# Kernel tuning notes

Measured on AMD Instinct MI355X. Metric: run time of the kernel, lower is better.

Reference implementation:

```python
import jax, jax.numpy as jnp
import numpy as np

MODEL_DIMS = 2048
BATCH, SEQ = 4, 4096
NFREQ = MODEL_DIMS // 2 + 1  # rfft spectrum length


def setup_inputs() -> dict:
    key = jax.random.key(0)
    k1, k2, k3, k4 = jax.random.split(key, 4)
    x = jax.random.normal(k1, (BATCH, SEQ, MODEL_DIMS), dtype=jnp.float32)
    queries = jax.random.normal(k2, (1, 1, NFREQ), dtype=jnp.float32)
    keyvalues = jax.random.normal(k3, (1, 1, NFREQ), dtype=jnp.float32)
    # torch nn.Linear(model_dims, model_dims, bias=False): weight is [out, in]
    w_out = jax.random.normal(k4, (MODEL_DIMS, MODEL_DIMS), dtype=jnp.float32) * (MODEL_DIMS ** -0.5)
    return {"x": x, "queries": queries, "keyvalues": keyvalues, "w_out": w_out}


def reference(x, queries, keyvalues, w_out):
    # hrr.fft = rfft over feature dim -> complex64 [B, S, NFREQ]
    xhat = jnp.fft.rfft(x, axis=-1)
    q = xhat * queries            # real spectral params broadcast-multiply
    kv = xhat * keyvalues
    kv = jnp.cumsum(kv, axis=1)   # causal prefix sum over sequence
    qv = q * kv
    values_hat = jnp.fft.irfft(qv, n=x.shape[-1], axis=-1)  # back to real [B, S, D]
    # torch Linear: y = x @ W^T
    return jnp.einsum('bsd,ed->bse', values_hat, w_out)
```

## Files before the change

kernel.cpp:

```cpp
#include <hip/hip_runtime.h>
#include <hip/hip_bf16.h>
#include <stdint.h>

#define BATCH 4
#define SEQ   4096
#define DIM   2048
#define NFREQ 1025
#define NCPLX 1024
#define ROWS  (BATCH*SEQ)

#define SCH  16
#define NSC  (SEQ/SCH)
#define NSCG 16
#define NGRP (NSC/NSCG)

#define SPEC_STRIDE 257

typedef __bf16 bf16x8 __attribute__((ext_vector_type(8)));
typedef float  f32x4  __attribute__((ext_vector_type(4)));

__device__ __forceinline__ int drev4(int n) {
  return ((n&3)<<8) | (((n>>2)&3)<<6) | (((n>>4)&3)<<4) | (((n>>6)&3)<<2) | ((n>>8)&3);
}
#define ZI(i) ((i) + ((i)>>4))

__device__ __forceinline__ float2 cmulf(float2 a, float2 b) {
  return make_float2(a.x*b.x - a.y*b.y, a.x*b.y + a.y*b.x);
}

__device__ __forceinline__ unsigned short f2bf(float f) {
  union { float f; unsigned u; } v; v.f = f;
  unsigned r = v.u + 0x7fffu + ((v.u >> 16) & 1u);
  return (unsigned short)(r >> 16);
}
__device__ __forceinline__ unsigned packbf(float2 v) {
  return (unsigned)f2bf(v.x) | ((unsigned)f2bf(v.y) << 16);
}
__device__ __forceinline__ float2 unpackbf(unsigned u) {
  union { unsigned u; float f; } a, b;
  a.u = u << 16; b.u = u & 0xffff0000u;
  return make_float2(a.f, b.f);
}

template<int INV>
__device__ __forceinline__ void fft_stages_tw(float2* z, int tid, const float2* tw1) {
  {
    int b4 = tid*4;
    float2 x0=z[ZI(b4)], x1=z[ZI(b4+1)], x2=z[ZI(b4+2)], x3=z[ZI(b4+3)];
    float2 a = make_float2(x0.x+x2.x, x0.y+x2.y), b = make_float2(x0.x-x2.x, x0.y-x2.y);
    float2 c = make_float2(x1.x+x3.x, x1.y+x3.y), d = make_float2(x1.x-x3.x, x1.y-x3.y);
    z[ZI(b4)]   = make_float2(a.x+c.x, a.y+c.y);
    z[ZI(b4+2)] = make_float2(a.x-c.x, a.y-c.y);
    if (!INV) { z[ZI(b4+1)] = make_float2(b.x+d.y, b.y-d.x);
                z[ZI(b4+3)] = make_float2(b.x-d.y, b.y+d.x); }
    else      { z[ZI(b4+1)] = make_float2(b.x-d.y, b.y+d.x);
                z[ZI(b4+3)] = make_float2(b.x+d.y, b.y-d.x); }
  }
  __syncthreads();
#pragma unroll
  for (int s = 0; s < 4; ++s) {
    const int lq = 2 + 2*s;
    const int q  = 1 << lq;
    int j = tid & (q-1), g = tid >> lq;
    int base = (g << (lq+2)) + j;
    float2 w1 = tw1[s]; if (INV) w1.y = -w1.y;
    float2 w2 = cmulf(w1, w1), w3 = cmulf(w2, w1);
    float2 x0 = z[ZI(base)];
    float2 x1 = cmulf(z[ZI(base+q)],   w1);
    float2 x2 = cmulf(z[ZI(base+2*q)], w2);
    float2 x3 = cmulf(z[ZI(base+3*q)], w3);
    float2 a = make_float2(x0.x+x2.x, x0.y+x2.y), b = make_float2(x0.x-x2.x, x0.y-x2.y);
    float2 c = make_float2(x1.x+x3.x, x1.y+x3.y), d = make_float2(x1.x-x3.x, x1.y-x3.y);
    z[ZI(base)]     = make_float2(a.x+c.x, a.y+c.y);
    z[ZI(base+2*q)] = make_float2(a.x-c.x, a.y-c.y);
    if (!INV) { z[ZI(base+q)]   = make_float2(b.x+d.y, b.y-d.x);
                z[ZI(base+3*q)] = make_float2(b.x-d.y, b.y+d.x); }
    else      { z[ZI(base+q)]   = make_float2(b.x-d.y, b.y+d.x);
                z[ZI(base+3*q)] = make_float2(b.x+d.y, b.y-d.x); }
    __syncthreads();
  }
}

__device__ __forceinline__ void make_tw1(int tid, float2* tw1) {
#pragma unroll
  for (int s = 0; s < 4; ++s) {
    const int lq = 2 + 2*s;
    const int q  = 1 << lq;
    int j = tid & (q-1);
    float ang = -6.2831853071795864769f * (float)j / (float)(4*q);
    float sw, cw; __sincosf(ang, &sw, &cw);
    tw1[s] = make_float2(cw, sw);
  }
}

__global__ __launch_bounds__(256) void fwd_fused(const float* __restrict__ x,
                                                 const float* __restrict__ kvs,
                                                 uint4* __restrict__ spec,
                                                 float2* __restrict__ partial) {
  __shared__ float2 z[ZI(1023)+2];
  const int tid = threadIdx.x;
  const int sc = blockIdx.x & (NSC-1), b = blockIdx.x >> 8;

  float2 tw1[4];
  make_tw1(tid, tw1);
  const int kA = tid, kB = tid + 256;
  float swA, cwA, swB, cwB;
  __sincosf(-3.14159265358979323846f * (float)kA / 1024.0f, &swA, &cwA);
  __sincosf(-3.14159265358979323846f * (float)kB / 1024.0f, &swB, &cwB);
  int id0 = ZI(drev4(2*tid)),     id1 = ZI(drev4(2*tid+1));
  int id2 = ZI(drev4(2*tid+512)), id3 = ZI(drev4(2*tid+513));

  float2 sA={0,0}, sAp={0,0}, sB={0,0}, sBp={0,0}, s5={0,0};

  const size_t row0 = (size_t)b*SEQ + (size_t)sc*SCH;
  const float* xrow = x + row0*DIM;
  float4 c0 = ((const float4*)xrow)[tid];
  float4 c1 = ((const float4*)xrow)[tid + 256];

  for (int s = 0; s < SCH; ++s) {
    float4 n0f, n1f;
    if (s+1 < SCH) {
      const float* nx = xrow + (size_t)(s+1)*DIM;
      n0f = ((const float4*)nx)[tid]; n1f = ((const float4*)nx)[tid + 256];
    }
    z[id0] = make_float2(c0.x, c0.y); z[id1] = make_float2(c0.z, c0.w);
    z[id2] = make_float2(c1.x, c1.y); z[id3] = make_float2(c1.z, c1.w);
    __syncthreads();
    fft_stages_tw<0>(z, tid, tw1);
    float2 ZkA = z[ZI(kA)], ZnA = z[ZI((NCPLX - kA) & (NCPLX-1))];
    float2 ZkB = z[ZI(kB)], ZnB = z[ZI(768 - tid)];
    float Er = 0.5f*(ZkA.x + ZnA.x), Ei = 0.5f*(ZkA.y - ZnA.y);
    float dr = 0.5f*(ZkA.x - ZnA.x), di = 0.5f*(ZkA.y + ZnA.y);
    float2 vA  = make_float2( Er + cwA*di + swA*dr,  Ei + swA*di - cwA*dr);
    float2 vAp = make_float2( Er - cwA*di - swA*dr, -Ei + swA*di - cwA*dr);
    float Fr = 0.5f*(ZkB.x + ZnB.x), Fi = 0.5f*(ZkB.y - ZnB.y);
    float er = 0.5f*(ZkB.x - ZnB.x), ei = 0.5f*(ZkB.y + ZnB.y);
    float2 vB  = make_float2( Fr + cwB*ei + swB*er,  Fi + swB*ei - cwB*er);
    float2 vBp = make_float2( Fr - cwB*ei - swB*er, -Fi + swB*ei - cwB*er);
    sA.x += vA.x;  sA.y += vA.y;   sAp.x += vAp.x; sAp.y += vAp.y;
    sB.x += vB.x;  sB.y += vB.y;   sBp.x += vBp.x; sBp.y += vBp.y;
    uint4* sprow = spec + (row0 + s) * SPEC_STRIDE;
    sprow[tid] = make_uint4(packbf(vA), packbf(vAp), packbf(vB), packbf(vBp));
    if (tid == 0) {
      float2 Z5 = z[ZI(512)];
      float2 v5 = make_float2(Z5.x, -Z5.y);
      s5.x += v5.x; s5.y += v5.y;
      ((unsigned*)(sprow + 256))[0] = packbf(v5);
    }
    __syncthreads();
    c0 = n0f; c1 = n1f;
  }
  float2* pp = partial + ((size_t)(b*NSC + sc)) * NFREQ;
  float kvA = kvs[kA], kvAp = kvs[NCPLX - kA], kvB = kvs[kB], kvBp = kvs[768 - tid];
  pp[kA]          = make_float2(kvA*sA.x,  kvA*sA.y);
  pp[NCPLX - kA]  = make_float2(kvAp*sAp.x, kvAp*sAp.y);
  pp[kB]          = make_float2(kvB*sB.x,  kvB*sB.y);
  pp[768 - tid]   = make_float2(kvBp*sBp.x, kvBp*sBp.y);
  if (tid == 0) { float kv5 = kvs[512]; pp[512] = make_float2(kv5*s5.x, kv5*s5.y); }
}

__global__ __launch_bounds__(256) void wfft(const float* __restrict__ w,
                                            unsigned short* __restrict__ H) {
  __shared__ float2 z[ZI(1023)+2];
  __shared__ __align__(16) unsigned short hrow[2048];
  const int tid = threadIdx.x;
  const int e = blockIdx.x;

  float2 tw1[4];
  make_tw1(tid, tw1);
  const int kB = tid + 256;
  float swA, cwA, swB, cwB;
  __sincosf(-3.14159265358979323846f * (float)tid / 1024.0f, &swA, &cwA);
  __sincosf(-3.14159265358979323846f * (float)kB  / 1024.0f, &swB, &cwB);
  int id0 = ZI(drev4(2*tid)),     id1 = ZI(drev4(2*tid+1));
  int id2 = ZI(drev4(2*tid+512)), id3 = ZI(drev4(2*tid+513));

  const float* wr = w + (size_t)e * DIM;
  float4 c0 = ((const float4*)wr)[tid];
  float4 c1 = ((const float4*)wr)[tid + 256];
  z[id0] = make_float2(c0.x, c0.y); z[id1] = make_float2(c0.z, c0.w);
  z[id2] = make_float2(c1.x, c1.y); z[id3] = make_float2(c1.z, c1.w);
  __syncthreads();
  fft_stages_tw<0>(z, tid, tw1);

  float2 ZkA = z[ZI(tid)], ZnA = z[ZI((NCPLX - tid) & (NCPLX-1))];
  float2 ZkB = z[ZI(kB)],  ZnB = z[ZI(768 - tid)];
  float Er = 0.5f*(ZkA.x + ZnA.x), Ei = 0.5f*(ZkA.y - ZnA.y);
  float dr = 0.5f*(ZkA.x - ZnA.x), di = 0.5f*(ZkA.y + ZnA.y);
  float2 vA  = make_float2( Er + cwA*di + swA*dr,  Ei + swA*di - cwA*dr);
  float2 vAp = make_float2( Er - cwA*di - swA*dr, -Ei + swA*di - cwA*dr);
  float Fr = 0.5f*(ZkB.x + ZnB.x), Fi = 0.5f*(ZkB.y - ZnB.y);
  float er = 0.5f*(ZkB.x - ZnB.x), ei = 0.5f*(ZkB.y + ZnB.y);
  float2 vB  = make_float2( Fr + cwB*ei + swB*er,  Fi + swB*ei - cwB*er);
  float2 vBp = make_float2( Fr - cwB*ei - swB*er, -Fi + swB*ei - cwB*er);

  const float invN = 1.0f/2048.0f, twoN = 2.0f/2048.0f;
  float aA  = (tid == 0) ? invN : twoN;
  float aAp = (tid == 0) ? invN : twoN;
  hrow[tid]        = f2bf(aA  * vA.x);
  hrow[1024 - tid] = f2bf(aAp * vAp.x);
  hrow[256 + tid]  = f2bf(twoN * vB.x);
  hrow[768 - tid]  = f2bf(twoN * vBp.x);
  if (tid) {
    hrow[1024 + tid] = f2bf(twoN * vA.y);
    hrow[2048 - tid] = f2bf(twoN * vAp.y);
  }
  hrow[1280 + tid] = f2bf(twoN * vB.y);
  hrow[1792 - tid] = f2bf(twoN * vBp.y);
  if (tid == 0) {
    float2 Z5 = z[ZI(512)];
    hrow[512]  = f2bf(twoN * Z5.x);
    hrow[1536] = f2bf(twoN * (-Z5.y));
  }
  __syncthreads();
  ((uint4*)(H + (size_t)e * DIM))[tid] = ((const uint4*)hrow)[tid];
}

__global__ __launch_bounds__(256) void scanA(float2* __restrict__ partial,
                                             float2* __restrict__ gtot) {
  int kc = blockIdx.x % 5, g = (blockIdx.x / 5) % NGRP, b = blockIdx.x / (5*NGRP);
  int k = kc*256 + threadIdx.x;
  if (k >= NFREQ) return;
  float2* p = partial + ((size_t)(b*NSC + g*NSCG)) * NFREQ + k;
  float2 run = {0.f, 0.f};
#pragma unroll
  for (int i = 0; i < NSCG; ++i) {
    float2 t = p[(size_t)i*NFREQ];
    p[(size_t)i*NFREQ] = run;
    run.x += t.x; run.y += t.y;
  }
  gtot[((size_t)(b*NGRP + g)) * NFREQ + k] = run;
}

__global__ __launch_bounds__(256) void scanB(float2* __restrict__ gtot) {
  int kc = blockIdx.x % 5, b = blockIdx.x / 5;
  int k = kc*256 + threadIdx.x;
  if (k >= NFREQ) return;
  float2* p = gtot + ((size_t)b*NGRP) * NFREQ + k;
  float2 run = {0.f, 0.f};
#pragma unroll
  for (int g = 0; g < NGRP; ++g) {
    float2 t = p[(size_t)g*NFREQ];
    p[(size_t)g*NFREQ] = run;
    run.x += t.x; run.y += t.y;
  }
}

__global__ __launch_bounds__(256) void inv_fused(const uint4* __restrict__ spec,
                                                 const float* __restrict__ kvs,
                                                 const float* __restrict__ qs_,
                                                 const float2* __restrict__ partial,
                                                 const float2* __restrict__ gtot,
                                                 unsigned short* __restrict__ G) {
  __shared__ __align__(16) unsigned short grow[2048];
  const int tid = threadIdx.x;
  const int sc = blockIdx.x & (NSC-1), b = blockIdx.x >> 8;
  const int kA = tid, kB = tid + 256;

  float ksA = kvs[kA], ksAp = kvs[NCPLX - kA], ksB = kvs[kB], ksBp = kvs[768 - tid];
  float qsA = qs_[kA], qsAp = qs_[NCPLX - kA], qsB = qs_[kB], qsBp = qs_[768 - tid];

  const float2* pp = partial + ((size_t)(b*NSC + sc)) * NFREQ;
  const float2* gp = gtot + ((size_t)(b*NGRP + (sc >> 4))) * NFREQ;
  float2 CA  = make_float2(pp[kA].x + gp[kA].x,                 pp[kA].y + gp[kA].y);
  float2 CAp = make_float2(pp[NCPLX-kA].x + gp[NCPLX-kA].x,     pp[NCPLX-kA].y + gp[NCPLX-kA].y);
  float2 CB  = make_float2(pp[kB].x + gp[kB].x,                 pp[kB].y + gp[kB].y);
  float2 CBp = make_float2(pp[768-tid].x + gp[768-tid].x,       pp[768-tid].y + gp[768-tid].y);
  float ks5 = kvs[512], qs5 = qs_[512];
  float2 C5 = make_float2(pp[512].x + gp[512].x, pp[512].y + gp[512].y);

  const size_t row0 = (size_t)b*SEQ + (size_t)sc*SCH;
  const uint4* sprow = spec + row0 * SPEC_STRIDE;
  uint4 sp = sprow[tid];
  unsigned spN = ((const unsigned*)(sprow + 256))[0];

  for (int s = 0; s < SCH; ++s) {
    uint4 spn; unsigned spNn;
    if (s+1 < SCH) {
      const uint4* nr = sprow + (size_t)(s+1) * SPEC_STRIDE;
      spn = nr[tid]; spNn = ((const unsigned*)(nr + 256))[0];
    }
    float2 vA = unpackbf(sp.x), vAp = unpackbf(sp.y);
    float2 vB = unpackbf(sp.z), vBp = unpackbf(sp.w);
    CA.x  += vA.x*ksA;   CA.y  += vA.y*ksA;
    CAp.x += vAp.x*ksAp; CAp.y += vAp.y*ksAp;
    CB.x  += vB.x*ksB;   CB.y  += vB.y*ksB;
    CBp.x += vBp.x*ksBp; CBp.y += vBp.y*ksBp;
    float2 qvA  = make_float2(qsA *(vA.x*CA.x  - vA.y*CA.y),  qsA *(vA.x*CA.y  + vA.y*CA.x));
    float2 qvAp = make_float2(qsAp*(vAp.x*CAp.x- vAp.y*CAp.y),qsAp*(vAp.x*CAp.y+ vAp.y*CAp.x));
    float2 qvB  = make_float2(qsB *(vB.x*CB.x  - vB.y*CB.y),  qsB *(vB.x*CB.y  + vB.y*CB.x));
    float2 qvBp = make_float2(qsBp*(vBp.x*CBp.x- vBp.y*CBp.y),qsBp*(vBp.x*CBp.y+ vBp.y*CBp.x));
    grow[tid]        = f2bf(qvA.x);
    grow[1024 - tid] = f2bf(qvAp.x);
    grow[256 + tid]  = f2bf(qvB.x);
    grow[768 - tid]  = f2bf(qvBp.x);
    if (tid) {
      grow[1024 + tid] = f2bf(qvA.y);
      grow[2048 - tid] = f2bf(qvAp.y);
    }
    grow[1280 + tid] = f2bf(qvB.y);
    grow[1792 - tid] = f2bf(qvBp.y);
    if (tid == 0) {
      float2 v5 = unpackbf(spN);
      C5.x += v5.x*ks5; C5.y += v5.y*ks5;
      grow[512]  = f2bf(qs5*(v5.x*C5.x - v5.y*C5.y));
      grow[1536] = f2bf(qs5*(v5.x*C5.y + v5.y*C5.x));
    }
    __syncthreads();
    ((uint4*)(G + (row0 + s) * DIM))[tid] = ((const uint4*)grow)[tid];
    __syncthreads();
    sp = spn; spN = spNn;
  }
}

#define NKT (DIM/64)
#define NIT (NKT/2)

#define BARX() do{ __builtin_amdgcn_s_barrier(); __builtin_amdgcn_sched_barrier(0); }while(0)
#define VMW(N) do{ asm volatile("s_waitcnt vmcnt(" #N ")" ::: "memory"); __builtin_amdgcn_sched_barrier(0); }while(0)

#define LOADA(B_, MH) do{ _Pragma("unroll") for (int m_=0;m_<4;++m_) _Pragma("unroll") for (int kk_=0;kk_<2;++kk_){ \
    int rA_ = wm*64 + m_*16 + l15; \
    aF[m_][kk_] = *(const bf16x8*)(smem + ((B_)*2+(MH))*16384 + rA_*128 + ((kk_*64 + lhi*16) ^ ((rA_&7)<<4))); } }while(0)

#define LOADB(DST, B_, NH) do{ _Pragma("unroll") for (int n_=0;n_<2;++n_) _Pragma("unroll") for (int kk_=0;kk_<2;++kk_){ \
    int rB_ = wn*32 + n_*16 + l15; \
    DST[n_][kk_] = *(const bf16x8*)(smem + 65536 + ((B_)*2+(NH))*16384 + rB_*128 + ((kk_*64 + lhi*16) ^ ((rB_&7)<<4))); } }while(0)

#define MM(MH, NH, BF) do{ __builtin_amdgcn_s_setprio(1); \
    _Pragma("unroll") for (int kk_=0;kk_<2;++kk_) _Pragma("unroll") for (int m_=0;m_<4;++m_) _Pragma("unroll") for (int n_=0;n_<2;++n_) \
      acc[MH][NH][m_][n_] = __builtin_amdgcn_mfma_f32_16x16x32_bf16(aF[m_][kk_], BF[n_][kk_], acc[MH][NH][m_][n_], 0, 0, 0); \
    __builtin_amdgcn_s_setprio(0); }while(0)

#define STAGEH(REG, B_, H_, GP, ROW0, KT) do{ _Pragma("unroll") for (int c_=0;c_<2;++c_){ \
    int ci_ = c_*512 + tid; int r_ = ci_>>3, sl_ = ci_&7; \
    const unsigned short* sp_ = (GP) + (size_t)((ROW0) + (H_)*128 + r_)*DIM + (KT) + ((sl_ ^ (r_&7))*8); \
    __builtin_amdgcn_global_load_lds((const __attribute__((address_space(1))) void*)sp_, \
      (__attribute__((address_space(3))) void*)(smem + (REG) + ((B_)*2+(H_))*16384 + ci_*16), 16, 0, 0); } }while(0)

__global__ __launch_bounds__(512, 2) void gemm256(const unsigned short* __restrict__ A,
                                                  const unsigned short* __restrict__ B,
                                                  float* __restrict__ C) {
  __shared__ __align__(16) char smem[131072];
  const int tid = threadIdx.x;
  const int lane = tid & 63;
  const int wid  = tid >> 6;
  const int wm = wid >> 2, wn = wid & 3;
  const int l15 = lane & 15, lhi = lane >> 4;

  const int xj = blockIdx.x & 7, tt = blockIdx.x >> 3;
  const int bm = xj * 8 + (tt >> 3), bn = tt & 7;
  const int m0 = bm * 256, n0 = bn * 256;

  f32x4 acc[2][2][4][2] = {};
  bf16x8 aF[4][2], bF0[2][2], bF1[2][2];

  STAGEH(0,     0,0, A, m0, 0);  STAGEH(65536, 0,0, B, n0, 0);
  STAGEH(65536, 0,1, B, n0, 0);  STAGEH(0,     0,1, A, m0, 0);
  STAGEH(0,     1,0, A, m0, 64); STAGEH(65536, 1,0, B, n0, 64);
  STAGEH(65536, 1,1, B, n0, 64); STAGEH(0,     1,1, A, m0, 64);
  VMW(8);
  BARX();

#pragma unroll 1
  for (int j = 0; j < NIT-1; ++j) {
    const int kA = (2*j+2)*64, kB = (2*j+3)*64;
    LOADA(0,0); LOADB(bF0, 0,0);
    BARX(); MM(0,0,bF0); BARX();
    LOADB(bF1, 0,1);
    STAGEH(0, 0,0, A, m0, kA); STAGEH(65536, 0,0, B, n0, kA);
    BARX(); MM(0,1,bF1); BARX();
    LOADA(0,1);
    STAGEH(65536, 0,1, B, n0, kA);
    BARX(); MM(1,0,bF0); BARX();
    STAGEH(0, 0,1, A, m0, kA);
    VMW(8);
    BARX(); MM(1,1,bF1); BARX();
    LOADA(1,0); LOADB(bF0, 1,0);
    BARX(); MM(0,0,bF0); BARX();
    LOADB(bF1, 1,1);
    STAGEH(0, 1,0, A, m0, kB); STAGEH(65536, 1,0, B, n0, kB);
    BARX(); MM(0,1,bF1); BARX();
    LOADA(1,1);
    STAGEH(65536, 1,1, B, n0, kB);
    BARX(); MM(1,0,bF0); BARX();
    STAGEH(0, 1,1, A, m0, kB);
    VMW(8);
    BARX(); MM(1,1,bF1); BARX();
  }
  LOADA(0,0); LOADB(bF0, 0,0);
  BARX(); MM(0,0,bF0); BARX();
  LOADB(bF1, 0,1);
  BARX(); MM(0,1,bF1); BARX();
  LOADA(0,1);
  BARX(); MM(1,0,bF0); BARX();
  VMW(0);
  BARX(); MM(1,1,bF1); BARX();
  LOADA(1,0); LOADB(bF0, 1,0);
  BARX(); MM(0,0,bF0); BARX();
  LOADB(bF1, 1,1);
  BARX(); MM(0,1,bF1); BARX();
  LOADA(1,1);
  BARX(); MM(1,0,bF0); BARX();
  BARX(); MM(1,1,bF1); BARX();

  const int crow = lhi * 4;
#pragma unroll
  for (int mh = 0; mh < 2; ++mh)
#pragma unroll
    for (int nh = 0; nh < 2; ++nh)
#pragma unroll
      for (int m_ = 0; m_ < 4; ++m_)
#pragma unroll
        for (int n_ = 0; n_ < 2; ++n_) {
          float* cp = C + (size_t)(m0 + mh*128 + wm*64 + m_*16 + crow) * DIM
                        + (n0 + nh*128 + wn*32 + n_*16 + l15);
#pragma unroll
          for (int j2 = 0; j2 < 4; ++j2)
            cp[(size_t)j2 * DIM] = acc[mh][nh][m_][n_][j2];
        }
}

extern "C" void kernel_launch(void* const* d_in, const int* in_sizes, int n_in,
                              void* d_out, int out_size, void* d_ws, size_t ws_size,
                              hipStream_t stream) {
  const float* x    = (const float*)d_in[0];
  const float* qry  = (const float*)d_in[1];
  const float* kvs  = (const float*)d_in[2];
  const float* wout = (const float*)d_in[3];
  float* out = (float*)d_out;

  char* ws = (char*)d_ws;
  size_t off = 0;
  uint4* spec = (uint4*)(ws + off);
  off += (size_t)ROWS * SPEC_STRIDE * sizeof(uint4);
  off = (off + 255) & ~(size_t)255;
  unsigned short* G = (unsigned short*)(ws + off);
  off += (size_t)ROWS * DIM * sizeof(unsigned short);
  off = (off + 255) & ~(size_t)255;
  unsigned short* H = (unsigned short*)(ws + off);
  off += (size_t)DIM * DIM * sizeof(unsigned short);
  off = (off + 255) & ~(size_t)255;
  float2* partial = (float2*)(ws + off);
  off += (size_t)BATCH * NSC * NFREQ * sizeof(float2);
  off = (off + 255) & ~(size_t)255;
  float2* gtot = (float2*)(ws + off);
  off += (size_t)BATCH * NGRP * NFREQ * sizeof(float2);

  hipLaunchKernelGGL(wfft,      dim3(DIM),               dim3(256), 0, stream, wout, H);
  hipLaunchKernelGGL(fwd_fused, dim3(BATCH*NSC),         dim3(256), 0, stream, x, kvs, spec, partial);
  hipLaunchKernelGGL(scanA,     dim3(BATCH*NGRP*5),      dim3(256), 0, stream, partial, gtot);
  hipLaunchKernelGGL(scanB,     dim3(BATCH*5),           dim3(256), 0, stream, gtot);
  hipLaunchKernelGGL(inv_fused, dim3(BATCH*NSC),         dim3(256), 0, stream, spec, kvs, qry, partial, gtot, G);
  hipLaunchKernelGGL(gemm256,   dim3((ROWS/256)*(DIM/256)), dim3(512), 0, stream, G, H, out);
}
```

Baseline: 222.9 us.

## Merge weight FFT into forward kernel and fold second-level scan into inverse

The separate weight-FFT kernel is folded into the forward spectral kernel as extra blocks in the same grid, so one launch covers both. The scanB kernel is removed: each inverse block now sums the group totals of all earlier groups itself. This cuts two kernel launches and their serialization gaps, and lets the weight FFT blocks fill the GPU alongside the forward blocks. In exchange, the inverse kernel does redundant reads of up to 15 group-total rows per block, and the merged kernel's shared memory footprint grows by the hrow buffer for every block.

```diff
diff --git a/kernel.cpp b/kernel.cpp
--- a/kernel.cpp
+++ b/kernel.cpp
@@ -93,22 +93,70 @@
   }
 }
 
-__global__ __launch_bounds__(256) void fwd_fused(const float* __restrict__ x,
-                                                 const float* __restrict__ kvs,
-                                                 uint4* __restrict__ spec,
-                                                 float2* __restrict__ partial) {
+__global__ __launch_bounds__(256) void fwd_wfft(const float* __restrict__ x,
+                                                const float* __restrict__ w,
+                                                const float* __restrict__ kvs,
+                                                uint4* __restrict__ spec,
+                                                float2* __restrict__ partial,
+                                                unsigned short* __restrict__ H) {
   __shared__ float2 z[ZI(1023)+2];
+  __shared__ __align__(16) unsigned short hrow[2048];
   const int tid = threadIdx.x;
-  const int sc = blockIdx.x & (NSC-1), b = blockIdx.x >> 8;
 
   float2 tw1[4];
   make_tw1(tid, tw1);
   const int kA = tid, kB = tid + 256;
+  int id0 = ZI(drev4(2*tid)),     id1 = ZI(drev4(2*tid+1));
+  int id2 = ZI(drev4(2*tid+512)), id3 = ZI(drev4(2*tid+513));
+
+  if (blockIdx.x >= BATCH*NSC) {
+    const int e = blockIdx.x - BATCH*NSC;
+    float swA, cwA, swB, cwB;
+    __sincosf(-3.14159265358979323846f * (float)kA / 1024.0f, &swA, &cwA);
+    __sincosf(-3.14159265358979323846f * (float)kB / 1024.0f, &swB, &cwB);
+    const float* wr = w + (size_t)e * DIM;
+    float4 c0 = ((const float4*)wr)[tid];
+    float4 c1 = ((const float4*)wr)[tid + 256];
+    z[id0] = make_float2(c0.x, c0.y); z[id1] = make_float2(c0.z, c0.w);
+    z[id2] = make_float2(c1.x, c1.y); z[id3] = make_float2(c1.z, c1.w);
+    __syncthreads();
+    fft_stages_tw<0>(z, tid, tw1);
+    float2 ZkA = z[ZI(kA)], ZnA = z[ZI((NCPLX - kA) & (NCPLX-1))];
+    float2 ZkB = z[ZI(kB)], ZnB = z[ZI(768 - tid)];
+    float Er = 0.5f*(ZkA.x + ZnA.x), Ei = 0.5f*(ZkA.y - ZnA.y);
+    float dr = 0.5f*(ZkA.x - ZnA.x), di = 0.5f*(ZkA.y + ZnA.y);
+    float2 vA  = make_float2( Er + cwA*di + swA*dr,  Ei + swA*di - cwA*dr);
+    float2 vAp = make_float2( Er - cwA*di - swA*dr, -Ei + swA*di - cwA*dr);
+    float Fr = 0.5f*(ZkB.x + ZnB.x), Fi = 0.5f*(ZkB.y - ZnB.y);
+    float er = 0.5f*(ZkB.x - ZnB.x), ei = 0.5f*(ZkB.y + ZnB.y);
+    float2 vB  = make_float2( Fr + cwB*ei + swB*er,  Fi + swB*ei - cwB*er);
+    float2 vBp = make_float2( Fr - cwB*ei - swB*er, -Fi + swB*ei - cwB*er);
+    const float invN = 1.0f/2048.0f, twoN = 2.0f/2048.0f;
+    float aA  = (tid == 0) ? invN : twoN;
+    hrow[tid]        = f2bf(aA   * vA.x);
+    hrow[1024 - tid] = f2bf(aA   * vAp.x);
+    hrow[256 + tid]  = f2bf(twoN * vB.x);
+    hrow[768 - tid]  = f2bf(twoN * vBp.x);
+    if (tid) {
+      hrow[1024 + tid] = f2bf(twoN * vA.y);
+      hrow[2048 - tid] = f2bf(twoN * vAp.y);
+    }
+    hrow[1280 + tid] = f2bf(twoN * vB.y);
+    hrow[1792 - tid] = f2bf(twoN * vBp.y);
+    if (tid == 0) {
+      float2 Z5 = z[ZI(512)];
+      hrow[512]  = f2bf(twoN * Z5.x);
+      hrow[1536] = f2bf(twoN * (-Z5.y));
+    }
+    __syncthreads();
+    ((uint4*)(H + (size_t)e * DIM))[tid] = ((const uint4*)hrow)[tid];
+    return;
+  }
+
+  const int sc = blockIdx.x & (NSC-1), b = blockIdx.x >> 8;
   float swA, cwA, swB, cwB;
   __sincosf(-3.14159265358979323846f * (float)kA / 1024.0f, &swA, &cwA);
   __sincosf(-3.14159265358979323846f * (float)kB / 1024.0f, &swB, &cwB);
-  int id0 = ZI(drev4(2*tid)),     id1 = ZI(drev4(2*tid+1));
-  int id2 = ZI(drev4(2*tid+512)), id3 = ZI(drev4(2*tid+513));
 
   float2 sA={0,0}, sAp={0,0}, sB={0,0}, sBp={0,0}, s5={0,0};
 
@@ -159,63 +207,6 @@
   if (tid == 0) { float kv5 = kvs[512]; pp[512] = make_float2(kv5*s5.x, kv5*s5.y); }
 }
 
-__global__ __launch_bounds__(256) void wfft(const float* __restrict__ w,
-                                            unsigned short* __restrict__ H) {
-  __shared__ float2 z[ZI(1023)+2];
-  __shared__ __align__(16) unsigned short hrow[2048];
-  const int tid = threadIdx.x;
-  const int e = blockIdx.x;
-
-  float2 tw1[4];
-  make_tw1(tid, tw1);
-  const int kB = tid + 256;
-  float swA, cwA, swB, cwB;
-  __sincosf(-3.14159265358979323846f * (float)tid / 1024.0f, &swA, &cwA);
-  __sincosf(-3.14159265358979323846f * (float)kB  / 1024.0f, &swB, &cwB);
-  int id0 = ZI(drev4(2*tid)),     id1 = ZI(drev4(2*tid+1));
-  int id2 = ZI(drev4(2*tid+512)), id3 = ZI(drev4(2*tid+513));
-
-  const float* wr = w + (size_t)e * DIM;
-  float4 c0 = ((const float4*)wr)[tid];
-  float4 c1 = ((const float4*)wr)[tid + 256];
-  z[id0] = make_float2(c0.x, c0.y); z[id1] = make_float2(c0.z, c0.w);
-  z[id2] = make_float2(c1.x, c1.y); z[id3] = make_float2(c1.z, c1.w);
-  __syncthreads();
-  fft_stages_tw<0>(z, tid, tw1);
-
-  float2 ZkA = z[ZI(tid)], ZnA = z[ZI((NCPLX - tid) & (NCPLX-1))];
-  float2 ZkB = z[ZI(kB)],  ZnB = z[ZI(768 - tid)];
-  float Er = 0.5f*(ZkA.x + ZnA.x), Ei = 0.5f*(ZkA.y - ZnA.y);
-  float dr = 0.5f*(ZkA.x - ZnA.x), di = 0.5f*(ZkA.y + ZnA.y);
-  float2 vA  = make_float2( Er + cwA*di + swA*dr,  Ei + swA*di - cwA*dr);
-  float2 vAp = make_float2( Er - cwA*di - swA*dr, -Ei + swA*di - cwA*dr);
-  float Fr = 0.5f*(ZkB.x + ZnB.x), Fi = 0.5f*(ZkB.y - ZnB.y);
-  float er = 0.5f*(ZkB.x - ZnB.x), ei = 0.5f*(ZkB.y + ZnB.y);
-  float2 vB  = make_float2( Fr + cwB*ei + swB*er,  Fi + swB*ei - cwB*er);
-  float2 vBp = make_float2( Fr - cwB*ei - swB*er, -Fi + swB*ei - cwB*er);
-
-  const float invN = 1.0f/2048.0f, twoN = 2.0f/2048.0f;
-  float aA  = (tid == 0) ? invN : twoN;
-  float aAp = (tid == 0) ? invN : twoN;
-  hrow[tid]        = f2bf(aA  * vA.x);
-  hrow[1024 - tid] = f2bf(aAp * vAp.x);
-  hrow[256 + tid]  = f2bf(twoN * vB.x);
-  hrow[768 - tid]  = f2bf(twoN * vBp.x);
-  if (tid) {
-    hrow[1024 + tid] = f2bf(twoN * vA.y);
-    hrow[2048 - tid] = f2bf(twoN * vAp.y);
-  }
-  hrow[1280 + tid] = f2bf(twoN * vB.y);
-  hrow[1792 - tid] = f2bf(twoN * vBp.y);
-  if (tid == 0) {
-    float2 Z5 = z[ZI(512)];
-    hrow[512]  = f2bf(twoN * Z5.x);
-    hrow[1536] = f2bf(twoN * (-Z5.y));
-  }
-  __syncthreads();
-  ((uint4*)(H + (size_t)e * DIM))[tid] = ((const uint4*)hrow)[tid];
-}
-
 __global__ __launch_bounds__(256) void scanA(float2* __restrict__ partial,
                                              float2* __restrict__ gtot) {
   int kc = blockIdx.x % 5, g = (blockIdx.x / 5) % NGRP, b = blockIdx.x / (5*NGRP);
@@ -230,20 +221,6 @@
     run.x += t.x; run.y += t.y;
   }
   gtot[((size_t)(b*NGRP + g)) * NFREQ + k] = run;
-}
-
-__global__ __launch_bounds__(256) void scanB(float2* __restrict__ gtot) {
-  int kc = blockIdx.x % 5, b = blockIdx.x / 5;
-  int k = kc*256 + threadIdx.x;
-  if (k >= NFREQ) return;
-  float2* p = gtot + ((size_t)b*NGRP) * NFREQ + k;
-  float2 run = {0.f, 0.f};
-#pragma unroll
-  for (int g = 0; g < NGRP; ++g) {
-    float2 t = p[(size_t)g*NFREQ];
-    p[(size_t)g*NFREQ] = run;
-    run.x += t.x; run.y += t.y;
-  }
 }
 
 __global__ __launch_bounds__(256) void inv_fused(const uint4* __restrict__ spec,
@@ -261,13 +238,20 @@
   float qsA = qs_[kA], qsAp = qs_[NCPLX - kA], qsB = qs_[kB], qsBp = qs_[768 - tid];
 
   const float2* pp = partial + ((size_t)(b*NSC + sc)) * NFREQ;
-  const float2* gp = gtot + ((size_t)(b*NGRP + (sc >> 4))) * NFREQ;
-  float2 CA  = make_float2(pp[kA].x + gp[kA].x,                 pp[kA].y + gp[kA].y);
-  float2 CAp = make_float2(pp[NCPLX-kA].x + gp[NCPLX-kA].x,     pp[NCPLX-kA].y + gp[NCPLX-kA].y);
-  float2 CB  = make_float2(pp[kB].x + gp[kB].x,                 pp[kB].y + gp[kB].y);
-  float2 CBp = make_float2(pp[768-tid].x + gp[768-tid].x,       pp[768-tid].y + gp[768-tid].y);
+  float2 CA  = pp[kA], CAp = pp[NCPLX-kA], CB = pp[kB], CBp = pp[768-tid];
   float ks5 = kvs[512], qs5 = qs_[512];
-  float2 C5 = make_float2(pp[512].x + gp[512].x, pp[512].y + gp[512].y);
+  float2 C5 = pp[512];
+  {
+    const int g = sc >> 4;
+    const float2* gb = gtot + (size_t)b*NGRP*NFREQ;
+    for (int gg = 0; gg < g; ++gg) {
+      const float2* gr = gb + (size_t)gg*NFREQ;
+      float2 a0 = gr[kA], a1 = gr[NCPLX-kA], a2 = gr[kB], a3 = gr[768-tid];
+      CA.x += a0.x; CA.y += a0.y;   CAp.x += a1.x; CAp.y += a1.y;
+      CB.x += a2.x; CB.y += a2.y;   CBp.x += a3.x; CBp.y += a3.y;
+      if (tid == 0) { float2 a5 = gr[512]; C5.x += a5.x; C5.y += a5.y; }
+    }
+  }
 
   const size_t row0 = (size_t)b*SEQ + (size_t)sc*SCH;
   const uint4* sprow = spec + row0 * SPEC_STRIDE;
@@ -447,10 +431,8 @@
   float2* gtot = (float2*)(ws + off);
   off += (size_t)BATCH * NGRP * NFREQ * sizeof(float2);
 
-  hipLaunchKernelGGL(wfft,      dim3(DIM),               dim3(256), 0, stream, wout, H);
-  hipLaunchKernelGGL(fwd_fused, dim3(BATCH*NSC),         dim3(256), 0, stream, x, kvs, spec, partial);
+  hipLaunchKernelGGL(fwd_wfft,  dim3(BATCH*NSC + DIM),   dim3(256), 0, stream, x, wout, kvs, spec, partial, H);
   hipLaunchKernelGGL(scanA,     dim3(BATCH*NGRP*5),      dim3(256), 0, stream, partial, gtot);
-  hipLaunchKernelGGL(scanB,     dim3(BATCH*5),           dim3(256), 0, stream, gtot);
   hipLaunchKernelGGL(inv_fused, dim3(BATCH*NSC),         dim3(256), 0, stream, spec, kvs, qry, partial, gtot, G);
   hipLaunchKernelGGL(gemm256,   dim3((ROWS/256)*(DIM/256)), dim3(512), 0, stream, G, H, out);
 }
```

New measurement: 223.5 us. Within noise of the previous version (+0.3%).
